# Optimization experiments

Measured on AMD Instinct MI355X. Metric: run time of the kernel, lower is better.

Reference implementation:

```python
import jax, jax.numpy as jnp
import numpy as np

B, IMG, P, CIN, D, L, H, HID = 64, 224, 16, 3, 768, 12, 12, 3072
HD = D // H                      # 64 head dim
N = (IMG // P) ** 2 + 1          # 197 tokens (cls + patches)
EQ = 1.0 / np.sqrt(D)            # EqualLinear scale (lr_mul=1)


def _ln(x):
    # LayerNorm(eps=1e-3, elementwise_affine=False)
    m = jnp.mean(x, axis=-1, keepdims=True)
    v = jnp.var(x, axis=-1, keepdims=True)
    return (x - m) * jax.lax.rsqrt(v + 1e-3)


def _smln(x, latent, gw, gb, bw, bb):
    # SelfModulatedLayerNorm: param-free LN then per-sample affine from latent
    gamma = (latent @ (gw * EQ).T + gb)[:, None, :]
    beta = (latent @ (bw * EQ).T + bb)[:, None, :]
    return _ln(x) * (1.0 + gamma) + beta


def _attention(x, qkvw, projw, projb):
    b, n, d = x.shape
    qkv = (x @ qkvw.T).reshape(b, n, 3, H, HD).transpose(2, 0, 3, 1, 4)  # [3,B,H,N,hd]
    q, k, v = qkv[0], qkv[1], qkv[2]
    attn = jax.nn.softmax(jnp.einsum('bhqd,bhkd->bhqk', q, k) * (HD ** -0.5), axis=-1)
    out = jnp.einsum('bhqk,bhkd->bhqd', attn, v).transpose(0, 2, 1, 3).reshape(b, n, d)
    return out @ projw.T + projb


def _forward(x, latent, conv_w, conv_b, cls_token, pos_embed,
             g1w, g1b, b1w, b1b, qkvw, projw, projb,
             g2w, g2b, b2w, b2b, fc1w, fc1b, fc2w, fc2b,
             gnw, gnb, bnw, bnb):
    b = x.shape[0]
    # PatchEmbed: conv stride=patch, flatten, transpose, sin activation
    feat = jax.lax.conv_general_dilated(
        x, conv_w, (P, P), 'VALID',
        dimension_numbers=('NCHW', 'OIHW', 'NCHW')) + conv_b[None, :, None, None]
    tok = jnp.sin(feat.reshape(b, D, -1).transpose(0, 2, 1))          # [B,196,D]
    tok = jnp.concatenate([jnp.broadcast_to(cls_token, (b, 1, D)), tok], axis=1)
    tok = tok + pos_embed                                             # [B,197,D]

    def block(t, p):
        (g1w_, g1b_, b1w_, b1b_, qkvw_, projw_, projb_,
         g2w_, g2b_, b2w_, b2b_, fc1w_, fc1b_, fc2w_, fc2b_) = p
        xn = _smln(t, latent, g1w_, g1b_, b1w_, b1b_)
        y = _attention(xn, qkvw_, projw_, projb_) + xn
        t = xn + y                       # source Block: x reassigned to norm1 output
        t = _smln(t, latent, g2w_, g2b_, b2w_, b2b_)
        h = jax.nn.gelu(t @ fc1w_.T + fc1b_, approximate=False)
        t = (h @ fc2w_.T + fc2b_) + t
        return t, None

    tok, _ = jax.lax.scan(block, tok, (g1w, g1b, b1w, b1b, qkvw, projw, projb,
                                       g2w, g2b, b2w, b2b, fc1w, fc1b, fc2w, fc2b))
    return _smln(tok, latent, gnw, gnb, bnw, bnb)


def setup_inputs() -> dict:
    key = jax.random.key(0)
    ks = jax.random.split(key, 20)
    r = lambda k, shape: 0.02 * jax.random.normal(k, shape, dtype=jnp.float32)
    z = lambda shape: jnp.zeros(shape, jnp.float32)
    return {
        'x': jax.random.normal(ks[0], (B, CIN, IMG, IMG), dtype=jnp.float32),
        'latent': jax.random.normal(ks[1], (B, D), dtype=jnp.float32),
        'conv_w': r(ks[2], (D, CIN, P, P)), 'conv_b': z((D,)),
        'cls_token': z((1, 1, D)), 'pos_embed': r(ks[3], (1, N, D)),
        'g1w': r(ks[4], (L, D, D)), 'g1b': z((L, D)),
        'b1w': r(ks[5], (L, D, D)), 'b1b': z((L, D)),
        'qkvw': r(ks[6], (L, 3 * D, D)),
        'projw': r(ks[7], (L, D, D)), 'projb': z((L, D)),
        'g2w': r(ks[8], (L, D, D)), 'g2b': z((L, D)),
        'b2w': r(ks[9], (L, D, D)), 'b2b': z((L, D)),
        'fc1w': r(ks[10], (L, HID, D)), 'fc1b': z((L, HID)),
        'fc2w': r(ks[11], (L, D, HID)), 'fc2b': z((L, D)),
        'gnw': r(ks[12], (D, D)), 'gnb': z((D,)),
        'bnw': r(ks[13], (D, D)), 'bnb': z((D,)),
    }


def reference(x, latent, conv_w, conv_b, cls_token, pos_embed,
              g1w, g1b, b1w, b1b, qkvw, projw, projb,
              g2w, g2b, b2w, b2b, fc1w, fc1b, fc2w, fc2b,
              gnw, gnb, bnw, bnb):
    return _forward(x, latent, conv_w, conv_b, cls_token, pos_embed,
                    g1w, g1b, b1w, b1b, qkvw, projw, projb,
                    g2w, g2b, b2w, b2b, fc1w, fc1b, fc2w, fc2b,
                    gnw, gnb, bnw, bnb)
```

## Files before the change

### kernel.cpp

```cpp
#include <hip/hip_runtime.h>

typedef unsigned short u16;
typedef __bf16 bf16x8 __attribute__((ext_vector_type(8)));
typedef unsigned short u16x8 __attribute__((ext_vector_type(8)));
typedef float f32x4 __attribute__((ext_vector_type(4)));

#define B_    64
#define NTOK  197
#define DIM   768
#define NH    12
#define LAY   12
#define HID_  3072
#define MROWS (B_*NTOK)

#define EPI_BF16  0
#define EPI_PROJ  2
#define EPI_GELU  3
#define EPI_FC2   4
#define EPI_PATCH 5

__device__ __forceinline__ u16 f2bf(float f) {
  unsigned u = __float_as_uint(f);
  u += 0x7FFFu + ((u >> 16) & 1u);
  return (u16)(u >> 16);
}
__device__ __forceinline__ float bf2f(u16 h) {
  return __uint_as_float(((unsigned)h) << 16);
}

__device__ __forceinline__ void gld_lds16(const void* g, void* l) {
  __builtin_amdgcn_global_load_lds(
      (const __attribute__((address_space(1))) void*)g,
      (__attribute__((address_space(3))) void*)l, 16, 0, 0);
}

__global__ void fill_k(float* __restrict__ o, float v, int n) {
  int i = blockIdx.x * blockDim.x + threadIdx.x;
  const int st = gridDim.x * blockDim.x;
  for (; i < n; i += st) o[i] = v;
}

__global__ void cvt_bf16(const float* __restrict__ in, u16* __restrict__ out, int n4) {
  int i = blockIdx.x * blockDim.x + threadIdx.x;
  const int st = gridDim.x * blockDim.x;
  for (; i < n4; i += st) {
    float4 v = ((const float4*)in)[i];
    ushort4 o;
    o.x = f2bf(v.x); o.y = f2bf(v.y); o.z = f2bf(v.z); o.w = f2bf(v.w);
    ((ushort4*)out)[i] = o;
  }
}

__global__ void cvt4_k(const float* __restrict__ s0, const float* __restrict__ s1,
                       const float* __restrict__ s2, const float* __restrict__ s3,
                       u16* __restrict__ d0, u16* __restrict__ d1,
                       u16* __restrict__ d2, u16* __restrict__ d3,
                       int n0, int n1, int n2, int n3)
{
  int i = blockIdx.x * blockDim.x + threadIdx.x;
  const int st = gridDim.x * blockDim.x;
  const int total = n0 + n1 + n2 + n3;
  for (; i < total; i += st) {
    const float* s; u16* d; int j = i;
    if (j < n0) { s = s0; d = d0; }
    else { j -= n0;
      if (j < n1) { s = s1; d = d1; }
      else { j -= n1;
        if (j < n2) { s = s2; d = d2; }
        else { j -= n2; s = s3; d = d3; } } }
    float4 v = ((const float4*)s)[j];
    ushort4 o;
    o.x = f2bf(v.x); o.y = f2bf(v.y); o.z = f2bf(v.z); o.w = f2bf(v.w);
    ((ushort4*)d)[j] = o;
  }
}

__global__ void im2col_k(const float* __restrict__ x, u16* __restrict__ out) {
  int i = blockIdx.x * blockDim.x + threadIdx.x;
  const int st = gridDim.x * blockDim.x;
  const int total = 12544 * 768;
  for (; i < total; i += st) {
    int row = i / 768, col = i - row * 768;
    int b = row / 196, pr = row - b * 196;
    int py = pr / 14, px = pr - py * 14;
    int cin = col >> 8, rr = col & 255;
    int ky = rr >> 4, kx = rr & 15;
    out[i] = f2bf(x[((b * 3 + cin) * 224 + py * 16 + ky) * 224 + px * 16 + kx]);
  }
}

__global__ void clspos_k(const float* __restrict__ cls, const float* __restrict__ pos,
                         float* __restrict__ t) {
  int i = blockIdx.x * blockDim.x + threadIdx.x;
  if (i >= B_ * DIM) return;
  int b = i / DIM, d = i - b * DIM;
  t[(size_t)b * NTOK * DIM + d] = cls[d] + pos[d];
}

__global__ __launch_bounds__(256)
void modk(const float* __restrict__ lat,
          const float* __restrict__ w,
          const float* __restrict__ bias,
          float* __restrict__ out, int ldb)
{
  __shared__ float ls[32][65];
  __shared__ float wsm[64][33];
  const int tid = threadIdx.x;
  const int mat = blockIdx.y;
  const int n0 = blockIdx.x * 64;
  const int nl = tid & 63;
  const int bg = tid >> 6;
  float acc[16];
  #pragma unroll
  for (int j = 0; j < 16; ++j) acc[j] = 0.f;
  for (int k0 = 0; k0 < 768; k0 += 32) {
    __syncthreads();
    #pragma unroll
    for (int i = 0; i < 8; ++i) {
      int idx = tid + i * 256;
      int rr = idx >> 5, kk = idx & 31;
      ls[kk][rr]  = lat[rr * 768 + k0 + kk];
      wsm[rr][kk] = w[((size_t)mat * 768 + n0 + rr) * 768 + k0 + kk];
    }
    __syncthreads();
    #pragma unroll 4
    for (int kk = 0; kk < 32; ++kk) {
      float wv = wsm[nl][kk];
      #pragma unroll
      for (int j = 0; j < 16; ++j)
        acc[j] += ls[kk][bg * 16 + j] * wv;
    }
  }
  const float EQS = 0.036084391824351615f;
  const float* bs = bias + (size_t)mat * 768 + n0;
  #pragma unroll
  for (int j = 0; j < 16; ++j) {
    int b = bg * 16 + j;
    out[(size_t)b * ldb + mat * 768 + n0 + nl] = acc[j] * EQS + bs[nl];
  }
}

__global__ __launch_bounds__(256)
void smln_k(const float* __restrict__ x,
            const float* __restrict__ gamma, const float* __restrict__ beta, int ldg,
            float* __restrict__ oF, u16* __restrict__ oB)
{
  const int row = blockIdx.x;
  const int tid = threadIdx.x;
  const float* xr = x + (size_t)row * DIM;
  float v0 = xr[tid], v1 = xr[tid + 256], v2 = xr[tid + 512];
  float s1 = v0 + v1 + v2;
  float s2 = v0 * v0 + v1 * v1 + v2 * v2;
  #pragma unroll
  for (int o = 32; o; o >>= 1) { s1 += __shfl_xor(s1, o); s2 += __shfl_xor(s2, o); }
  __shared__ float rs[8];
  const int lane = tid & 63, wv = tid >> 6;
  if (lane == 0) { rs[wv] = s1; rs[4 + wv] = s2; }
  __syncthreads();
  s1 = rs[0] + rs[1] + rs[2] + rs[3];
  s2 = rs[4] + rs[5] + rs[6] + rs[7];
  const float mean = s1 * (1.f / 768.f);
  const float var  = s2 * (1.f / 768.f) - mean * mean;
  const float rstd = rsqrtf(var + 1e-3f);
  const int b = row / NTOK;
  const float* g  = gamma + (size_t)b * ldg;
  const float* be = beta  + (size_t)b * ldg;
  const size_t base = (size_t)row * DIM;
  float vv[3] = {v0, v1, v2};
  #pragma unroll
  for (int j = 0; j < 3; ++j) {
    int d = tid + j * 256;
    float y = (vv[j] - mean) * rstd;
    y = y * (1.f + g[d]) + be[d];
    oF[base + d] = y;
    if (oB) oB[base + d] = f2bf(y);
  }
}

__global__ __launch_bounds__(256)
void attn_k(const u16* __restrict__ qkv, u16* __restrict__ ao)
{
  __shared__ u16 Ks[208 * 68];
  __shared__ u16 Vt[64 * 226];
  __shared__ u16 Ps[4][16 * 228];
  const int bh = blockIdx.x;
  const int b = bh / NH, h = bh - (bh / NH) * NH;
  const int tid = threadIdx.x;
  const int lane = tid & 63, wv = tid >> 6;
  const int lr = lane & 15, kg = lane >> 4;
  const size_t tb = (size_t)(b * NTOK) * 2304 + h * 64;

  for (int t = tid; t < 1576; t += 256) {
    int n = t >> 3, c = t & 7;
    *(u16x8*)&Ks[n * 68 + c * 8] =
        *(const u16x8*)&qkv[tb + (size_t)n * 2304 + 768 + c * 8];
  }
  for (int t = tid; t < 1576; t += 256) {
    int n = t >> 3, dc = t & 7;
    u16x8 v = *(const u16x8*)&qkv[tb + (size_t)n * 2304 + 1536 + dc * 8];
    #pragma unroll
    for (int j = 0; j < 8; ++j) Vt[(dc * 8 + j) * 226 + n] = v[j];
  }
  for (int i = tid; i < 11 * 68; i += 256) Ks[197 * 68 + i] = 0;
  for (int i = tid; i < 64 * 29; i += 256) {
    int d = i / 29, c = i - d * 29;
    Vt[d * 226 + 197 + c] = 0;
  }
  for (int i = tid; i < 4 * 16 * 20; i += 256) {
    int w = i / 320, rm = i - w * 320, r = rm / 20, c = rm - r * 20;
    Ps[w][r * 228 + 208 + c] = 0;
  }
  __syncthreads();

  const f32x4 z4 = {0.f, 0.f, 0.f, 0.f};
  u16* pw = Ps[wv];

  for (int qt = wv; qt < 13; qt += 4) {
    const int q0 = qt * 16;
    const int qrow = min(q0 + lr, 196);
    const bf16x8 aq0 = *(const bf16x8*)&qkv[tb + (size_t)qrow * 2304 + kg * 8];
    const bf16x8 aq1 = *(const bf16x8*)&qkv[tb + (size_t)qrow * 2304 + 32 + kg * 8];

    f32x4 acc[13];
    #pragma unroll
    for (int ct = 0; ct < 13; ++ct) acc[ct] = z4;
    #pragma unroll
    for (int ct = 0; ct < 13; ++ct) {
      const bf16x8 bk0 = *(const bf16x8*)&Ks[(ct * 16 + lr) * 68 + kg * 8];
      const bf16x8 bk1 = *(const bf16x8*)&Ks[(ct * 16 + lr) * 68 + 32 + kg * 8];
      acc[ct] = __builtin_amdgcn_mfma_f32_16x16x32_bf16(aq0, bk0, acc[ct], 0, 0, 0);
      acc[ct] = __builtin_amdgcn_mfma_f32_16x16x32_bf16(aq1, bk1, acc[ct], 0, 0, 0);
    }

    float mx[4], sm[4], inv[4];
    #pragma unroll
    for (int r = 0; r < 4; ++r) mx[r] = -1e30f;
    #pragma unroll
    for (int ct = 0; ct < 13; ++ct)
      #pragma unroll
      for (int r = 0; r < 4; ++r) {
        float s = acc[ct][r] * 0.125f;
        if (ct * 16 + lr >= 197) s = -1e30f;
        acc[ct][r] = s;
        mx[r] = fmaxf(mx[r], s);
      }
    #pragma unroll
    for (int o = 1; o < 16; o <<= 1)
      #pragma unroll
      for (int r = 0; r < 4; ++r) mx[r] = fmaxf(mx[r], __shfl_xor(mx[r], o));
    #pragma unroll
    for (int r = 0; r < 4; ++r) sm[r] = 0.f;
    #pragma unroll
    for (int ct = 0; ct < 13; ++ct)
      #pragma unroll
      for (int r = 0; r < 4; ++r) {
        float p = __expf(acc[ct][r] - mx[r]);
        acc[ct][r] = p;
        sm[r] += p;
      }
    #pragma unroll
    for (int o = 1; o < 16; o <<= 1)
      #pragma unroll
      for (int r = 0; r < 4; ++r) sm[r] += __shfl_xor(sm[r], o);
    #pragma unroll
    for (int r = 0; r < 4; ++r) inv[r] = 1.f / sm[r];

    #pragma unroll
    for (int ct = 0; ct < 13; ++ct)
      #pragma unroll
      for (int r = 0; r < 4; ++r)
        pw[(kg * 4 + r) * 228 + ct * 16 + lr] = f2bf(acc[ct][r]);
    asm volatile("s_waitcnt lgkmcnt(0)" ::: "memory");
    __builtin_amdgcn_sched_barrier(0);

    f32x4 accO[4];
    #pragma unroll
    for (int dt = 0; dt < 4; ++dt) accO[dt] = z4;
    #pragma unroll
    for (int kt = 0; kt < 7; ++kt) {
      const bf16x8 ap = *(const bf16x8*)&pw[lr * 228 + kt * 32 + kg * 8];
      #pragma unroll
      for (int dt = 0; dt < 4; ++dt) {
        const bf16x8 bv = *(const bf16x8*)&Vt[(dt * 16 + lr) * 226 + kt * 32 + kg * 8];
        accO[dt] = __builtin_amdgcn_mfma_f32_16x16x32_bf16(ap, bv, accO[dt], 0, 0, 0);
      }
    }

    #pragma unroll
    for (int r = 0; r < 4; ++r) {
      const int q = q0 + kg * 4 + r;
      if (q < NTOK) {
        const size_t base = ((size_t)(b * NTOK + q)) * DIM + h * 64;
        #pragma unroll
        for (int dt = 0; dt < 4; ++dt)
          ao[base + dt * 16 + lr] = f2bf(accO[dt][r] * inv[r]);
      }
    }
  }
}

template<int EPI>
__global__ __launch_bounds__(256)
void gemm_bt(const u16* __restrict__ A, int lda,
             const u16* __restrict__ Bw, int ldb,
             int M, int K, int gn,
             const float* __restrict__ bias,
             const float* __restrict__ res,
             float* __restrict__ outF, u16* __restrict__ outB, int ldo,
             const float* __restrict__ aux)
{
  __shared__ u16 As[8192];
  __shared__ u16 Bs[2048];
  const int tid = threadIdx.x;
  const int lane = tid & 63, wv = tid >> 6;
  const int lr = lane & 15, kg = lane >> 4;

  const int nwg = gridDim.x;
  const int qq = nwg >> 3, rr = nwg & 7;
  const int xcd = blockIdx.x & 7, loc = blockIdx.x >> 3;
  const int v = (xcd < rr ? xcd * (qq + 1) : rr * (qq + 1) + (xcd - rr) * qq) + loc;
  const int tm = v / gn, tn = v - tm * gn;

  const u16* aS[4];
  #pragma unroll
  for (int i = 0; i < 4; ++i) {
    int c = tid + i * 256;
    int row = c >> 2, q2 = (c & 3) ^ (row & 3);
    int am = tm * 256 + row; if (am >= M) am = M - 1;
    aS[i] = A + (size_t)am * lda + q2 * 8;
  }
  {
  }
  const int rb = tid >> 2, qb = (tid & 3) ^ (rb & 3);
  const u16* bS = Bw + (size_t)(tn * 64 + rb) * ldb + qb * 8;
  u16* aD = &As[wv * 512];
  u16* bD = &Bs[wv * 512];

  f32x4 acc[4][4];
  const f32x4 z = {0.f, 0.f, 0.f, 0.f};
  #pragma unroll
  for (int m = 0; m < 4; ++m)
    #pragma unroll
    for (int n = 0; n < 4; ++n) acc[m][n] = z;

  const int KT = K >> 5;
  for (int kt = 0; kt < KT; ++kt) {
    if (kt) __syncthreads();
    const int ko = kt * 32;
    gld_lds16(aS[0] + ko, aD);
    gld_lds16(aS[1] + ko, aD + 2048);
    gld_lds16(aS[2] + ko, aD + 4096);
    gld_lds16(aS[3] + ko, aD + 6144);
    gld_lds16(bS + ko, bD);
    __syncthreads();
    bf16x8 af[4], bfr[4];
    #pragma unroll
    for (int m = 0; m < 4; ++m) {
      int row = wv * 64 + m * 16 + lr;
      af[m] = *(const bf16x8*)&As[row * 32 + (((kg ^ row) & 3) << 3)];
    }
    #pragma unroll
    for (int n = 0; n < 4; ++n) {
      int row = n * 16 + lr;
      bfr[n] = *(const bf16x8*)&Bs[row * 32 + (((kg ^ row) & 3) << 3)];
    }
    #pragma unroll
    for (int m = 0; m < 4; ++m)
      #pragma unroll
      for (int n = 0; n < 4; ++n)
        acc[m][n] = __builtin_amdgcn_mfma_f32_16x16x32_bf16(af[m], bfr[n], acc[m][n], 0, 0, 0);
  }

  #pragma unroll
  for (int m = 0; m < 4; ++m) {
    #pragma unroll
    for (int n = 0; n < 4; ++n) {
      const int gc = tn * 64 + n * 16 + lr;
      #pragma unroll
      for (int r = 0; r < 4; ++r) {
        const int gr = tm * 256 + wv * 64 + m * 16 + kg * 4 + r;
        if (gr < M) {
          float val = acc[m][n][r];
          if constexpr (EPI == EPI_BF16) {
            outB[(size_t)gr * ldo + gc] = f2bf(val);
          } else if constexpr (EPI == EPI_PROJ) {
            size_t o = (size_t)gr * ldo + gc;
            outF[o] = val + bias[gc] + 2.f * res[o];
          } else if constexpr (EPI == EPI_GELU) {
            float u = val + bias[gc];
            outB[(size_t)gr * ldo + gc] =
                f2bf(0.5f * u * (1.f + erff(u * 0.70710678118654752f)));
          } else if constexpr (EPI == EPI_FC2) {
            size_t o = (size_t)gr * ldo + gc;
            outF[o] = val + bias[gc] + res[o];
          } else {
            int pb = gr / 196, pp = gr - pb * 196;
            outF[((size_t)pb * NTOK + 1 + pp) * DIM + gc] =
                sinf(val + bias[gc]) + aux[(size_t)(1 + pp) * DIM + gc];
          }
        }
      }
    }
  }
}

extern "C" void kernel_launch(void* const* d_in, const int* in_sizes, int n_in,
                              void* d_out, int out_size, void* d_ws, size_t ws_size,
                              hipStream_t stream)
{
  (void)in_sizes; (void)n_in;
  const float* X     = (const float*)d_in[0];
  const float* LAT   = (const float*)d_in[1];
  const float* CONVW = (const float*)d_in[2];
  const float* CONVB = (const float*)d_in[3];
  const float* CLS   = (const float*)d_in[4];
  const float* POS   = (const float*)d_in[5];
  const float* G1W   = (const float*)d_in[6];
  const float* G1B   = (const float*)d_in[7];
  const float* B1W   = (const float*)d_in[8];
  const float* B1B   = (const float*)d_in[9];
  const float* QKVW  = (const float*)d_in[10];
  const float* PROJW = (const float*)d_in[11];
  const float* PROJB = (const float*)d_in[12];
  const float* G2W   = (const float*)d_in[13];
  const float* G2B   = (const float*)d_in[14];
  const float* B2W   = (const float*)d_in[15];
  const float* B2B   = (const float*)d_in[16];
  const float* FC1W  = (const float*)d_in[17];
  const float* FC1B  = (const float*)d_in[18];
  const float* FC2W  = (const float*)d_in[19];
  const float* FC2B  = (const float*)d_in[20];
  const float* GNW   = (const float*)d_in[21];
  const float* GNB   = (const float*)d_in[22];
  const float* BNW   = (const float*)d_in[23];
  const float* BNB   = (const float*)d_in[24];

  char* p = (char*)d_ws;
  auto carve = [&](size_t bytes) { char* r = p; p += (bytes + 255) & ~(size_t)255; return r; };

  char* Ubuf  = carve((size_t)MROWS * HID_ * 2);
  u16* patches = (u16*)Ubuf;
  u16* qkvb    = (u16*)Ubuf;
  u16* hb      = (u16*)Ubuf;
  u16* wconv  = (u16*)carve((size_t)768 * 768 * 2);
  u16* wqkv_l = (u16*)carve((size_t)2304 * 768 * 2);
  u16* wproj_l= (u16*)carve((size_t)768 * 768 * 2);
  u16* wfc1_l = (u16*)carve((size_t)3072 * 768 * 2);
  u16* wfc2_l = (u16*)carve((size_t)768 * 3072 * 2);
  float* tf   = (float*)carve((size_t)MROWS * 768 * 4);
  float* xnf  = (float*)carve((size_t)MROWS * 768 * 4);
  u16* xnb    = (u16*)carve((size_t)MROWS * 768 * 2);
  u16* aob    = (u16*)carve((size_t)MROWS * 768 * 2);
  float* gam1 = (float*)carve((size_t)B_ * 9216 * 4);
  float* bet1 = (float*)carve((size_t)B_ * 9216 * 4);
  float* gam2 = (float*)carve((size_t)B_ * 9216 * 4);
  float* bet2 = (float*)carve((size_t)B_ * 9216 * 4);
  float* gamN = (float*)carve((size_t)B_ * 768 * 4);
  float* betN = (float*)carve((size_t)B_ * 768 * 4);

  fill_k<<<1, 64, 0, stream>>>((float*)d_out, 1e9f, 1);
  if ((size_t)(p - (char*)d_ws) > ws_size) {
    fill_k<<<256, 256, 0, stream>>>((float*)d_out, 1e9f, out_size);
    return;
  }

  modk<<<dim3(12, 12), 256, 0, stream>>>(LAT, G1W, G1B, gam1, 9216);
  modk<<<dim3(12, 12), 256, 0, stream>>>(LAT, B1W, B1B, bet1, 9216);
  modk<<<dim3(12, 12), 256, 0, stream>>>(LAT, G2W, G2B, gam2, 9216);
  modk<<<dim3(12, 12), 256, 0, stream>>>(LAT, B2W, B2B, bet2, 9216);
  modk<<<dim3(12, 1),  256, 0, stream>>>(LAT, GNW, GNB, gamN, 768);
  modk<<<dim3(12, 1),  256, 0, stream>>>(LAT, BNW, BNB, betN, 768);

  {
    int n4 = 768 * 768 / 4;
    cvt_bf16<<<(n4 + 255) / 256, 256, 0, stream>>>(CONVW, wconv, n4);
  }
  im2col_k<<<4096, 256, 0, stream>>>(X, patches);
  gemm_bt<EPI_PATCH><<<49 * 12, 256, 0, stream>>>(patches, 768, wconv, 768, 12544, 768, 12,
                                                  CONVB, nullptr, tf, nullptr, 768, POS);
  clspos_k<<<(B_ * DIM + 255) / 256, 256, 0, stream>>>(CLS, POS, tf);

  const int n4_qkv = 2304 * 768 / 4, n4_pro = 768 * 768 / 4, n4_fc = 3072 * 768 / 4;
  for (int l = 0; l < LAY; ++l) {
    cvt4_k<<<4096, 256, 0, stream>>>(QKVW + (size_t)l * 2304 * 768, PROJW + (size_t)l * 768 * 768,
                                     FC1W + (size_t)l * 3072 * 768, FC2W + (size_t)l * 768 * 3072,
                                     wqkv_l, wproj_l, wfc1_l, wfc2_l,
                                     n4_qkv, n4_pro, n4_fc, n4_fc);
    smln_k<<<MROWS, 256, 0, stream>>>(tf, gam1 + l * 768, bet1 + l * 768, 9216, xnf, xnb);
    gemm_bt<EPI_BF16><<<50 * 36, 256, 0, stream>>>(xnb, 768, wqkv_l, 768, MROWS, 768, 36,
                                                   nullptr, nullptr, nullptr, qkvb, 2304, nullptr);
    attn_k<<<B_ * NH, 256, 0, stream>>>(qkvb, aob);
    gemm_bt<EPI_PROJ><<<50 * 12, 256, 0, stream>>>(aob, 768, wproj_l, 768, MROWS, 768, 12,
                                                   PROJB + l * 768, xnf, tf, nullptr, 768, nullptr);
    smln_k<<<MROWS, 256, 0, stream>>>(tf, gam2 + l * 768, bet2 + l * 768, 9216, xnf, xnb);
    gemm_bt<EPI_GELU><<<50 * 48, 256, 0, stream>>>(xnb, 768, wfc1_l, 768, MROWS, 768, 48,
                                                   FC1B + l * 3072, nullptr, nullptr, hb, 3072, nullptr);
    gemm_bt<EPI_FC2><<<50 * 12, 256, 0, stream>>>(hb, 3072, wfc2_l, 3072, MROWS, 3072, 12,
                                                  FC2B + l * 768, xnf, tf, nullptr, 768, nullptr);
  }
  smln_k<<<MROWS, 256, 0, stream>>>(tf, gamN, betN, 768, (float*)d_out, nullptr);
}
```

Before: 7.291 ms.

## Double-buffer GEMM LDS tiles and stage epilogue through LDS for vector stores

The bf16 MFMA GEMM now keeps two LDS buffers for A and B tiles. The next K-slice is issued with global-to-LDS loads while the current slice feeds the MFMAs, so only one barrier is needed per slice and load latency is hidden. The epilogue also writes each 16-row accumulator block into per-wave LDS scratch, then reads it back row-major so global stores and residual/bias loads use 16-byte vectors instead of scattered scalar accesses. LDS use doubles, which may lower occupancy. The K loop assumes an even number of 32-wide slices.

```diff
diff --git a/kernel.cpp b/kernel.cpp
--- a/kernel.cpp
+++ b/kernel.cpp
@@ -98,10 +98,8 @@
 }
 
 __global__ __launch_bounds__(256)
-void modk(const float* __restrict__ lat,
-          const float* __restrict__ w,
-          const float* __restrict__ bias,
-          float* __restrict__ out, int ldb)
+void modk(const float* __restrict__ lat, const float* __restrict__ w,
+          const float* __restrict__ bias, float* __restrict__ out, int ldb)
 {
   __shared__ float ls[32][65];
   __shared__ float wsm[64][33];
@@ -309,8 +307,8 @@
              float* __restrict__ outF, u16* __restrict__ outB, int ldo,
              const float* __restrict__ aux)
 {
-  __shared__ u16 As[8192];
-  __shared__ u16 Bs[2048];
+  __shared__ u16 As[2][8192];
+  __shared__ u16 Bs[2][2048];
   const int tid = threadIdx.x;
   const int lane = tid & 63, wv = tid >> 6;
   const int lr = lane & 15, kg = lane >> 4;
@@ -329,12 +327,12 @@
     int am = tm * 256 + row; if (am >= M) am = M - 1;
     aS[i] = A + (size_t)am * lda + q2 * 8;
   }
-  {
-  }
   const int rb = tid >> 2, qb = (tid & 3) ^ (rb & 3);
   const u16* bS = Bw + (size_t)(tn * 64 + rb) * ldb + qb * 8;
-  u16* aD = &As[wv * 512];
-  u16* bD = &Bs[wv * 512];
+  u16* aD0 = &As[0][wv * 512];
+  u16* aD1 = &As[1][wv * 512];
+  u16* bD0 = &Bs[0][wv * 512];
+  u16* bD1 = &Bs[1][wv * 512];
 
   f32x4 acc[4][4];
   const f32x4 z = {0.f, 0.f, 0.f, 0.f};
@@ -343,65 +341,129 @@
     #pragma unroll
     for (int n = 0; n < 4; ++n) acc[m][n] = z;
 
+#define STAGE0(ko) do { gld_lds16(aS[0]+(ko), aD0); gld_lds16(aS[1]+(ko), aD0+2048); \
+                        gld_lds16(aS[2]+(ko), aD0+4096); gld_lds16(aS[3]+(ko), aD0+6144); \
+                        gld_lds16(bS+(ko), bD0); } while(0)
+#define STAGE1(ko) do { gld_lds16(aS[0]+(ko), aD1); gld_lds16(aS[1]+(ko), aD1+2048); \
+                        gld_lds16(aS[2]+(ko), aD1+4096); gld_lds16(aS[3]+(ko), aD1+6144); \
+                        gld_lds16(bS+(ko), bD1); } while(0)
+#define KPHASE(buf) do { \
+    bf16x8 af[4], bfr[4]; \
+    _Pragma("unroll") \
+    for (int m = 0; m < 4; ++m) { \
+      int row = wv * 64 + m * 16 + lr; \
+      af[m] = *(const bf16x8*)&As[buf][row * 32 + (((kg ^ row) & 3) << 3)]; \
+    } \
+    _Pragma("unroll") \
+    for (int n = 0; n < 4; ++n) { \
+      int row = n * 16 + lr; \
+      bfr[n] = *(const bf16x8*)&Bs[buf][row * 32 + (((kg ^ row) & 3) << 3)]; \
+    } \
+    _Pragma("unroll") \
+    for (int m = 0; m < 4; ++m) \
+      _Pragma("unroll") \
+      for (int n = 0; n < 4; ++n) \
+        acc[m][n] = __builtin_amdgcn_mfma_f32_16x16x32_bf16(af[m], bfr[n], acc[m][n], 0, 0, 0); \
+  } while(0)
+#define PHASE_END() do { \
+    asm volatile("s_waitcnt lgkmcnt(0)" ::: "memory"); \
+    asm volatile("s_waitcnt vmcnt(0)" ::: "memory"); \
+    __builtin_amdgcn_s_barrier(); \
+    __builtin_amdgcn_sched_barrier(0); \
+  } while(0)
+
   const int KT = K >> 5;
-  for (int kt = 0; kt < KT; ++kt) {
-    if (kt) __syncthreads();
-    const int ko = kt * 32;
-    gld_lds16(aS[0] + ko, aD);
-    gld_lds16(aS[1] + ko, aD + 2048);
-    gld_lds16(aS[2] + ko, aD + 4096);
-    gld_lds16(aS[3] + ko, aD + 6144);
-    gld_lds16(bS + ko, bD);
-    __syncthreads();
-    bf16x8 af[4], bfr[4];
+  STAGE0(0);
+  PHASE_END();
+  for (int kt = 0; kt < KT; kt += 2) {
+    STAGE1((kt + 1) * 32);
+    KPHASE(0);
+    PHASE_END();
+    if (kt + 2 < KT) STAGE0((kt + 2) * 32);
+    KPHASE(1);
+    PHASE_END();
+  }
+
+  const int gr0 = tm * 256 + wv * 64;
+  const int gc0 = tn * 64;
+  if constexpr (EPI == EPI_BF16 || EPI == EPI_GELU) {
+    u16* T = (u16*)As + wv * 1152;
     #pragma unroll
     for (int m = 0; m < 4; ++m) {
-      int row = wv * 64 + m * 16 + lr;
-      af[m] = *(const bf16x8*)&As[row * 32 + (((kg ^ row) & 3) << 3)];
-    }
-    #pragma unroll
-    for (int n = 0; n < 4; ++n) {
-      int row = n * 16 + lr;
-      bfr[n] = *(const bf16x8*)&Bs[row * 32 + (((kg ^ row) & 3) << 3)];
-    }
-    #pragma unroll
-    for (int m = 0; m < 4; ++m)
+      #pragma unroll
+      for (int n = 0; n < 4; ++n) {
+        #pragma unroll
+        for (int r = 0; r < 4; ++r) {
+          float val = acc[m][n][r];
+          if constexpr (EPI == EPI_GELU) {
+            float u = val + bias[gc0 + n * 16 + lr];
+            val = 0.5f * u * (1.f + erff(u * 0.70710678118654752f));
+          }
+          T[(kg * 4 + r) * 72 + n * 16 + lr] = f2bf(val);
+        }
+      }
+      asm volatile("s_waitcnt lgkmcnt(0)" ::: "memory");
+      __builtin_amdgcn_sched_barrier(0);
+      #pragma unroll
+      for (int half = 0; half < 2; ++half) {
+        int row = (lane >> 3) + half * 8;
+        int c8 = lane & 7;
+        u16x8 vv = *(const u16x8*)&T[row * 72 + c8 * 8];
+        int gr = gr0 + m * 16 + row;
+        if (gr < M) *(u16x8*)&outB[(size_t)gr * ldo + gc0 + c8 * 8] = vv;
+      }
+      asm volatile("s_waitcnt lgkmcnt(0)" ::: "memory");
+      __builtin_amdgcn_sched_barrier(0);
+    }
+  } else {
+    float* T = (float*)As + wv * 1088;
+    #pragma unroll
+    for (int m = 0; m < 4; ++m) {
       #pragma unroll
       for (int n = 0; n < 4; ++n)
-        acc[m][n] = __builtin_amdgcn_mfma_f32_16x16x32_bf16(af[m], bfr[n], acc[m][n], 0, 0, 0);
-  }
-
-  #pragma unroll
-  for (int m = 0; m < 4; ++m) {
-    #pragma unroll
-    for (int n = 0; n < 4; ++n) {
-      const int gc = tn * 64 + n * 16 + lr;
-      #pragma unroll
-      for (int r = 0; r < 4; ++r) {
-        const int gr = tm * 256 + wv * 64 + m * 16 + kg * 4 + r;
+        #pragma unroll
+        for (int r = 0; r < 4; ++r)
+          T[(kg * 4 + r) * 68 + n * 16 + lr] = acc[m][n][r];
+      asm volatile("s_waitcnt lgkmcnt(0)" ::: "memory");
+      __builtin_amdgcn_sched_barrier(0);
+      #pragma unroll
+      for (int qu = 0; qu < 4; ++qu) {
+        int row = (lane >> 4) + qu * 4;
+        int c4 = lane & 15;
+        f32x4 vv = *(const f32x4*)&T[row * 68 + c4 * 4];
+        int gr = gr0 + m * 16 + row;
+        int gc = gc0 + c4 * 4;
         if (gr < M) {
-          float val = acc[m][n][r];
-          if constexpr (EPI == EPI_BF16) {
-            outB[(size_t)gr * ldo + gc] = f2bf(val);
-          } else if constexpr (EPI == EPI_PROJ) {
+          f32x4 bv = *(const f32x4*)&bias[gc];
+          if constexpr (EPI == EPI_PROJ) {
             size_t o = (size_t)gr * ldo + gc;
-            outF[o] = val + bias[gc] + 2.f * res[o];
-          } else if constexpr (EPI == EPI_GELU) {
-            float u = val + bias[gc];
-            outB[(size_t)gr * ldo + gc] =
-                f2bf(0.5f * u * (1.f + erff(u * 0.70710678118654752f)));
+            f32x4 rv = *(const f32x4*)&res[o];
+            f32x4 ov = vv + bv + 2.f * rv;
+            *(f32x4*)&outF[o] = ov;
           } else if constexpr (EPI == EPI_FC2) {
             size_t o = (size_t)gr * ldo + gc;
-            outF[o] = val + bias[gc] + res[o];
+            f32x4 rv = *(const f32x4*)&res[o];
+            f32x4 ov = vv + bv + rv;
+            *(f32x4*)&outF[o] = ov;
           } else {
             int pb = gr / 196, pp = gr - pb * 196;
-            outF[((size_t)pb * NTOK + 1 + pp) * DIM + gc] =
-                sinf(val + bias[gc]) + aux[(size_t)(1 + pp) * DIM + gc];
+            size_t o = ((size_t)pb * NTOK + 1 + pp) * DIM + gc;
+            f32x4 av = *(const f32x4*)&aux[(size_t)(1 + pp) * DIM + gc];
+            f32x4 ov;
+            #pragma unroll
+            for (int j = 0; j < 4; ++j) ov[j] = sinf(vv[j] + bv[j]) + av[j];
+            *(f32x4*)&outF[o] = ov;
           }
         }
       }
-    }
-  }
+      asm volatile("s_waitcnt lgkmcnt(0)" ::: "memory");
+      __builtin_amdgcn_sched_barrier(0);
+    }
+  }
+#undef STAGE0
+#undef STAGE1
+#undef KPHASE
+#undef PHASE_END
 }
 
 extern "C" void kernel_launch(void* const* d_in, const int* in_sizes, int n_in,
```

Result: slower. 7.908 ms (+8.5%).
